# Performance work log

Measured on AMD Instinct MI355X. Metric: run time of the kernel, lower is better.

Reference implementation:

```python
import jax, jax.numpy as jnp
import numpy as np

CLASS_NUM = 20
C_FEAT = 256
STRIDE = 16
ROI = 7
SCALE = 1.0 / 16.0
TOPK = 300
NMS_THR = 0.7
SCORE_THR = 0.5
SAMPLES = 2  # nearest samples per bin edge in roi_pool


def _conv(x, W, b, stride, padding):
    y = jax.lax.conv_general_dilated(x, W, (stride, stride), padding,
                                     dimension_numbers=('NCHW', 'OIHW', 'NCHW'))
    return y + b[None, :, None, None]


def _pairwise_iou(boxes):
    x1, y1, x2, y2 = boxes[:, 0], boxes[:, 1], boxes[:, 2], boxes[:, 3]
    area = jnp.maximum(x2 - x1, 0.) * jnp.maximum(y2 - y1, 0.)
    ix1 = jnp.maximum(x1[:, None], x1[None, :])
    iy1 = jnp.maximum(y1[:, None], y1[None, :])
    ix2 = jnp.minimum(x2[:, None], x2[None, :])
    iy2 = jnp.minimum(y2[:, None], y2[None, :])
    inter = jnp.maximum(ix2 - ix1, 0.) * jnp.maximum(iy2 - iy1, 0.)
    return inter / jnp.maximum(area[:, None] + area[None, :] - inter, 1e-6)


def _nms(boxes, scores, valid, thr):
    # fixed-size greedy NMS: returns boolean keep mask aligned with input order
    K = boxes.shape[0]
    order = jnp.argsort(-scores)
    b = boxes[order]
    v = valid[order]
    iou = _pairwise_iou(b)  # [K,K]
    idx = jnp.arange(K)

    def body(i, keep):
        k = keep[i] & v[i]
        suppress = (iou[i] > thr) & (idx > i) & k
        return keep & (~suppress)

    keep = jax.lax.fori_loop(0, K, body, v)
    return jnp.zeros((K,), bool).at[order].set(keep)


def _roi_pool(f, boxes):
    # f: [C,H,W] feature map; boxes: [K,4] in image coords.
    # Max pool over ROI x SAMPLES nearest-neighbor samples per bin (jit-safe roi_pool).
    C, H, W = f.shape
    K = boxes.shape[0]
    b = boxes * SCALE
    frac = (jnp.arange(ROI)[:, None] + (jnp.arange(SAMPLES)[None, :] + 0.5) / SAMPLES).reshape(-1) / ROI
    xs = b[:, 0:1] + frac[None, :] * (b[:, 2:3] - b[:, 0:1])  # [K, ROI*S]
    ys = b[:, 1:2] + frac[None, :] * (b[:, 3:4] - b[:, 1:2])
    ix = jnp.clip(jnp.floor(xs), 0, W - 1).astype(jnp.int32)
    iy = jnp.clip(jnp.floor(ys), 0, H - 1).astype(jnp.int32)
    g = f[:, iy[:, :, None], ix[:, None, :]]  # [C,K,ROI*S,ROI*S]
    g = g.reshape(C, K, ROI, SAMPLES, ROI, SAMPLES)
    return g.max(axis=(3, 5)).transpose(1, 0, 2, 3)  # [K,C,ROI,ROI]


def setup_inputs() -> dict:
    key = jax.random.key(0)
    ks = jax.random.split(key, 12)
    img = 800
    x = jax.random.uniform(ks[0], (1, 3, img, img), jnp.float32)
    gt_boxes = jax.random.uniform(ks[1], (8, 5), jnp.float32) * img

    def w_(k, shape, fan_in):
        return jax.random.normal(k, shape, jnp.float32) * (1.0 / np.sqrt(fan_in))

    d_flat = ROI * ROI * C_FEAT
    return {
        'x': x, 'gt_boxes': gt_boxes,
        'W_feat': w_(ks[2], (C_FEAT, 3, STRIDE, STRIDE), 3 * STRIDE * STRIDE),
        'b_feat': jnp.zeros((C_FEAT,), jnp.float32),
        'W1': w_(ks[3], (C_FEAT, C_FEAT, 3, 3), C_FEAT * 9),
        'b1': jnp.zeros((C_FEAT,), jnp.float32),
        'Wc': w_(ks[4], (2, C_FEAT), C_FEAT),
        'bc': jnp.zeros((2,), jnp.float32),
        'Wb': w_(ks[5], (4, C_FEAT), C_FEAT),
        'bb': jnp.zeros((4,), jnp.float32),
        'fc1_w': w_(ks[6], (4096, d_flat), d_flat),
        'fc1_b': jnp.zeros((4096,), jnp.float32),
        'fc2_w': w_(ks[7], (4096, 4096), 4096),
        'fc2_b': jnp.zeros((4096,), jnp.float32),
        'cls_w': w_(ks[8], (CLASS_NUM + 1, 4096), 4096),
        'cls_b': jnp.zeros((CLASS_NUM + 1,), jnp.float32),
        'box_w': w_(ks[9], (4, 4096), 4096),
        'box_b': jnp.zeros((4,), jnp.float32),
        'w': 800, 'h': 800,
    }


def reference(x, gt_boxes, W_feat, b_feat, W1, b1, Wc, bc, Wb, bb,
              fc1_w, fc1_b, fc2_w, fc2_b, cls_w, cls_b, box_w, box_b, w, h):
    feature = _conv(x, W_feat, b_feat, STRIDE, 'VALID')          # [1,C,50,50]
    hmap = jax.nn.relu(_conv(feature, W1, b1, 1, 'SAME'))
    pre_labels = (jnp.einsum('nchw,oc->nhwo', hmap, Wc) + bc).reshape(-1, 2)
    pre_boxes = (jnp.einsum('nchw,oc->nhwo', hmap, Wb) + bb).reshape(-1, 4)
    logits = jax.nn.softmax(pre_labels, axis=-1)[:, 1]           # [2500]
    scores, idx = jax.lax.top_k(logits, TOPK)                    # fixed-size stand-in for score>thr select
    valid = scores > SCORE_THR
    pb = pre_boxes[idx]
    wf = jnp.float32(w)
    hf = jnp.float32(h)
    # box decode exactly as the original per-box loop (vectorized)
    x1 = jnp.maximum(pb[:, 2] - pb[:, 0] / 2, 0.)
    y1 = jnp.maximum(pb[:, 3] - pb[:, 1] / 2, 0.)
    x2 = jnp.minimum(pb[:, 2] + pb[:, 0], wf)
    y2 = jnp.minimum(pb[:, 3] + pb[:, 1], hf)
    boxes = jnp.stack([x1, y1, x2, y2], axis=-1)                 # [K,4]
    keep = _nms(boxes, scores, valid, NMS_THR)
    pooled = _roi_pool(feature[0], boxes)                        # [K,C,7,7]
    flat = pooled.reshape(TOPK, -1)
    h1 = jax.nn.relu(flat @ fc1_w.T + fc1_b)
    h2 = jax.nn.relu(h1 @ fc2_w.T + fc2_b)
    cls = h2 @ cls_w.T + cls_b                                   # [K,21]
    box = h2 @ box_w.T + box_b                                   # [K,4]
    out = jnp.where(keep[:, None], jnp.concatenate([cls, box], axis=-1), 0.)
    return out                                                   # [K,25]
```

## Files before the change

kernel.cpp:

```cpp
#include <hip/hip_runtime.h>
#include <hip/hip_bf16.h>
#include <math.h>

#define NPIX   2500
#define CFEAT  256
#define NTOP   300
#define DFLAT  12544
#define FCN    4096
#define FPSTRIDE 3328
#define KG1    392
#define KG2    128
#define MT     20

typedef _Float16 f16x8 __attribute__((ext_vector_type(8)));
typedef float    f32x4 __attribute__((ext_vector_type(4)));

static constexpr size_t OFF_FPAD  = 0;
static constexpr size_t OFF_HMAP  = 0x340000;
static constexpr size_t OFF_SCORE = 0x5C0000;
static constexpr size_t OFF_PREB  = 0x5D0000;
static constexpr size_t OFF_TS    = 0x5E0000;
static constexpr size_t OFF_TI    = 0x5E1000;
static constexpr size_t OFF_KEEP  = 0x5E5000;
static constexpr size_t OFF_IX    = 0x5E6000;
static constexpr size_t OFF_IY    = 0x5EB000;
static constexpr size_t OFF_AFRAG = 0x600000;
static constexpr size_t OFF_H1F   = 0xE00000;
static constexpr size_t OFF_H2    = 0x1100000;
static constexpr size_t OFF_W1T   = 0x1600000;
static constexpr size_t OFF_PART  = 0x1900000;

__device__ inline float decode_dim(const void* p) {
    int iv = *(const int*)p;
    if (iv > 0 && iv < (1 << 20)) return (float)iv;
    return __int_as_float(iv);
}

__global__ void zero_fpad(float* __restrict__ fpad) {
    int i = blockIdx.x * 256 + threadIdx.x;
    if (i < 212992) *(float4*)(fpad + (size_t)i * 4) = make_float4(0.f, 0.f, 0.f, 0.f);
}

__global__ void __launch_bounds__(256)
patch_conv(const float* __restrict__ x, const float* __restrict__ Wf,
           const float* __restrict__ bf, float* __restrict__ fpad) {
    __shared__ float w[3072];
    int co0 = blockIdx.y * 4;
    for (int t = threadIdx.x; t < 3072; t += 256) w[t] = Wf[co0 * 768 + t];
    __syncthreads();
    int p = blockIdx.x * 256 + threadIdx.x;
    if (p >= NPIX) return;
    int py = p / 50, px = p % 50;
    float acc[4];
    #pragma unroll
    for (int c = 0; c < 4; ++c) acc[c] = bf[co0 + c];
    for (int ci = 0; ci < 3; ++ci) {
        const float* xp = x + ci * 640000 + (py * 16) * 800 + px * 16;
        #pragma unroll
        for (int ky = 0; ky < 16; ++ky) {
            const float* row = xp + ky * 800;
            #pragma unroll
            for (int kq = 0; kq < 4; ++kq) {
                float4 xv = *reinterpret_cast<const float4*>(row + kq * 4);
                int kb = ci * 256 + ky * 16 + kq * 4;
                #pragma unroll
                for (int c = 0; c < 4; ++c) {
                    const float* wc = w + c * 768 + kb;
                    acc[c] += xv.x * wc[0] + xv.y * wc[1] + xv.z * wc[2] + xv.w * wc[3];
                }
            }
        }
    }
    size_t o = (size_t)(py + 1) * 64 + (px + 1);
    #pragma unroll
    for (int c = 0; c < 4; ++c) fpad[(size_t)(co0 + c) * FPSTRIDE + o] = acc[c];
}

__global__ void transpose_w1(const float* __restrict__ W1, float* __restrict__ W1t) {
    int idx = blockIdx.x * 256 + threadIdx.x;
    if (idx >= 2304 * 256) return;
    int r = idx >> 8, co = idx & 255;
    W1t[idx] = W1[co * 2304 + r];
}

__global__ void __launch_bounds__(256)
conv3x3_part(const float* __restrict__ fpad, const float* __restrict__ W1t,
             float* __restrict__ cpart) {
    int co = threadIdx.x;
    int xb = blockIdx.x * 8;
    int y  = blockIdx.y;
    int z  = blockIdx.z;
    float acc[8];
    #pragma unroll
    for (int p = 0; p < 8; ++p) acc[p] = 0.0f;
    const float* fp = fpad + (size_t)(z * 64) * FPSTRIDE + (size_t)y * 64 + xb;
    const float* wp = W1t + (size_t)(z * 64) * 9 * 256 + co;
    #pragma unroll 2
    for (int ci = 0; ci < 64; ++ci) {
        float v[3][12];
        #pragma unroll
        for (int dy = 0; dy < 3; ++dy) {
            #pragma unroll
            for (int q = 0; q < 3; ++q) {
                float4 r4 = *(const float4*)(fp + dy * 64 + q * 4);
                v[dy][q * 4 + 0] = r4.x; v[dy][q * 4 + 1] = r4.y;
                v[dy][q * 4 + 2] = r4.z; v[dy][q * 4 + 3] = r4.w;
            }
        }
        float wv[9];
        #pragma unroll
        for (int k = 0; k < 9; ++k) wv[k] = wp[k * 256];
        #pragma unroll
        for (int dy = 0; dy < 3; ++dy)
            #pragma unroll
            for (int dx = 0; dx < 3; ++dx) {
                float wvv = wv[dy * 3 + dx];
                #pragma unroll
                for (int p = 0; p < 8; ++p)
                    acc[p] += v[dy][p + dx] * wvv;
            }
        fp += FPSTRIDE;
        wp += 9 * 256;
    }
    size_t base = (size_t)z * (NPIX * 256) + (size_t)(y * 50 + xb) * 256 + co;
    #pragma unroll
    for (int p = 0; p < 8; ++p)
        if (xb + p < 50) cpart[base + (size_t)p * 256] = acc[p];
}

__global__ void reduce_conv(const float* __restrict__ cpart, const float* __restrict__ b1,
                            float* __restrict__ hmap) {
    int i = blockIdx.x * 256 + threadIdx.x;
    if (i >= NPIX * 256 / 4) return;
    float4 s = *(const float4*)(cpart + (size_t)i * 4);
    #pragma unroll
    for (int z = 1; z < 4; ++z) {
        float4 v = *(const float4*)(cpart + (size_t)z * (NPIX * 256) + (size_t)i * 4);
        s.x += v.x; s.y += v.y; s.z += v.z; s.w += v.w;
    }
    float4 b = *(const float4*)(b1 + (i & 63) * 4);
    s.x = fmaxf(s.x + b.x, 0.f); s.y = fmaxf(s.y + b.y, 0.f);
    s.z = fmaxf(s.z + b.z, 0.f); s.w = fmaxf(s.w + b.w, 0.f);
    *(float4*)(hmap + (size_t)i * 4) = s;
}

__global__ void head_k(const float* __restrict__ hmap, const float* __restrict__ Wc,
                       const float* __restrict__ bc, const float* __restrict__ Wb,
                       const float* __restrict__ bb, float* __restrict__ score,
                       float* __restrict__ preb) {
    int lane = threadIdx.x & 63;
    int p = blockIdx.x * 4 + (threadIdx.x >> 6);
    if (p >= NPIX) return;
    float4 h  = *(const float4*)(hmap + (size_t)p * 256 + lane * 4);
    float4 c0 = *(const float4*)(Wc + lane * 4);
    float4 c1 = *(const float4*)(Wc + 256 + lane * 4);
    float4 w0 = *(const float4*)(Wb + lane * 4);
    float4 w1 = *(const float4*)(Wb + 256 + lane * 4);
    float4 w2 = *(const float4*)(Wb + 512 + lane * 4);
    float4 w3 = *(const float4*)(Wb + 768 + lane * 4);
    float s[6];
    s[0] = h.x*c0.x + h.y*c0.y + h.z*c0.z + h.w*c0.w;
    s[1] = h.x*c1.x + h.y*c1.y + h.z*c1.z + h.w*c1.w;
    s[2] = h.x*w0.x + h.y*w0.y + h.z*w0.z + h.w*w0.w;
    s[3] = h.x*w1.x + h.y*w1.y + h.z*w1.z + h.w*w1.w;
    s[4] = h.x*w2.x + h.y*w2.y + h.z*w2.z + h.w*w2.w;
    s[5] = h.x*w3.x + h.y*w3.y + h.z*w3.z + h.w*w3.w;
    #pragma unroll
    for (int o = 1; o < 64; o <<= 1) {
        #pragma unroll
        for (int q = 0; q < 6; ++q) s[q] += __shfl_xor(s[q], o, 64);
    }
    if (lane == 0) {
        float s0 = s[0] + bc[0], s1 = s[1] + bc[1];
        float m = fmaxf(s0, s1);
        float e0 = expf(s0 - m), e1 = expf(s1 - m);
        score[p] = e1 / (e0 + e1);
        preb[p * 4 + 0] = s[2] + bb[0];
        preb[p * 4 + 1] = s[3] + bb[1];
        preb[p * 4 + 2] = s[4] + bb[2];
        preb[p * 4 + 3] = s[5] + bb[3];
    }
}

__global__ void __launch_bounds__(1024) topk_k(const float* __restrict__ score,
                                               float* __restrict__ ts, int* __restrict__ ti) {
    __shared__ float sv[4096];
    __shared__ int   si[4096];
    int tid = threadIdx.x;
    for (int t = tid; t < 4096; t += 1024) {
        sv[t] = (t < NPIX) ? score[t] : -INFINITY;
        si[t] = t;
    }
    __syncthreads();
    for (int k = 2; k <= 4096; k <<= 1) {
        for (int j = k >> 1; j > 0; j >>= 1) {
            for (int t = tid; t < 4096; t += 1024) {
                int l = t ^ j;
                if (l > t) {
                    float vt = sv[t], vl = sv[l];
                    int it = si[t], il = si[l];
                    bool l_before_t = (vl > vt) || (vl == vt && il < it);
                    bool dir = ((t & k) == 0);
                    if (dir == l_before_t) {
                        sv[t] = vl; sv[l] = vt;
                        si[t] = il; si[l] = it;
                    }
                }
            }
            __syncthreads();
        }
    }
    for (int t = tid; t < NTOP; t += 1024) { ts[t] = sv[t]; ti[t] = si[t]; }
}

__global__ void __launch_bounds__(320)
nms_fused(const float* __restrict__ preb, const int* __restrict__ ti,
          const float* __restrict__ ts, const void* wp_, const void* hp_,
          int* __restrict__ keep, int* __restrict__ ixb, int* __restrict__ iyb) {
    __shared__ float X1[320], Y1[320], X2[320], Y2[320], AR[320];
    __shared__ unsigned long long MASK[320][5];
    __shared__ unsigned long long KEEPW[5];
    int t = threadIdx.x;
    int lane = t & 63;
    int w = t >> 6;

    float x1 = 0.f, y1 = 0.f, x2 = 0.f, y2 = 0.f;
    bool v = false;
    if (t < NTOP) {
        float wf = decode_dim(wp_), hf = decode_dim(hp_);
        int id = ti[t];
        float p0 = preb[id * 4 + 0], p1 = preb[id * 4 + 1];
        float p2 = preb[id * 4 + 2], p3 = preb[id * 4 + 3];
        x1 = fmaxf(p2 - p0 * 0.5f, 0.0f);
        y1 = fmaxf(p3 - p1 * 0.5f, 0.0f);
        x2 = fminf(p2 + p0, wf);
        y2 = fminf(p3 + p1, hf);
        v = ts[t] > 0.5f;
        float bx1 = x1 * 0.0625f, by1 = y1 * 0.0625f;
        float bx2 = x2 * 0.0625f, by2 = y2 * 0.0625f;
        #pragma unroll
        for (int m = 0; m < 14; ++m) {
            int i = m >> 1, s = m & 1;
            float frac = ((float)i + (s ? 0.75f : 0.25f)) / 7.0f;
            float xs = bx1 + frac * (bx2 - bx1);
            float ys = by1 + frac * (by2 - by1);
            float fx = floorf(xs); fx = fminf(fmaxf(fx, 0.0f), 49.0f);
            float fy = floorf(ys); fy = fminf(fmaxf(fy, 0.0f), 49.0f);
            ixb[t * 14 + m] = (int)fx;
            iyb[t * 14 + m] = (int)fy;
        }
    }
    X1[t] = x1; Y1[t] = y1; X2[t] = x2; Y2[t] = y2;
    AR[t] = fmaxf(x2 - x1, 0.0f) * fmaxf(y2 - y1, 0.0f);
    unsigned long long vb = __ballot(v);
    if (lane == 0) KEEPW[w] = vb;
    __syncthreads();

    float xi1 = X1[t], yi1 = Y1[t], xi2 = X2[t], yi2 = Y2[t], ai = AR[t];
    #pragma unroll
    for (int jw = 0; jw < 5; ++jw) {
        unsigned long long mword = 0ull;
        #pragma unroll 4
        for (int j2 = 0; j2 < 64; ++j2) {
            int j = jw * 64 + j2;
            float ix1 = fmaxf(xi1, X1[j]);
            float iy1 = fmaxf(yi1, Y1[j]);
            float ix2 = fminf(xi2, X2[j]);
            float iy2 = fminf(yi2, Y2[j]);
            float inter = fmaxf(ix2 - ix1, 0.0f) * fmaxf(iy2 - iy1, 0.0f);
            float iou = inter / fmaxf(ai + AR[j] - inter, 1e-6f);
            bool sup = (iou > 0.7f) && (j > t) && (j < NTOP);
            mword |= sup ? (1ull << j2) : 0ull;
        }
        MASK[t][jw] = mword;
    }
    __syncthreads();
    if (w != 0) return;

    unsigned long long m[5][5];
    #pragma unroll
    for (int g = 0; g < 5; ++g)
        #pragma unroll
        for (int q = 0; q < 5; ++q)
            m[g][q] = MASK[g * 64 + lane][q];
    unsigned long long kw0 = KEEPW[0], kw1 = KEEPW[1], kw2 = KEEPW[2],
                       kw3 = KEEPW[3], kw4 = KEEPW[4];
    #pragma unroll
    for (int g = 0; g < 5; ++g) {
        for (int i2 = 0; i2 < 64; ++i2) {
            unsigned long long kg = (g == 0) ? kw0 : (g == 1) ? kw1 :
                                    (g == 2) ? kw2 : (g == 3) ? kw3 : kw4;
            bool alive = (kg >> i2) & 1ull;
            unsigned long long b0 = __shfl(m[g][0], i2, 64);
            unsigned long long b1 = __shfl(m[g][1], i2, 64);
            unsigned long long b2 = __shfl(m[g][2], i2, 64);
            unsigned long long b3 = __shfl(m[g][3], i2, 64);
            unsigned long long b4 = __shfl(m[g][4], i2, 64);
            if (alive) {
                kw0 &= ~b0; kw1 &= ~b1; kw2 &= ~b2; kw3 &= ~b3; kw4 &= ~b4;
            }
        }
    }
    #pragma unroll
    for (int g = 0; g < 5; ++g) {
        unsigned long long kg = (g == 0) ? kw0 : (g == 1) ? kw1 :
                                (g == 2) ? kw2 : (g == 3) ? kw3 : kw4;
        int j = g * 64 + lane;
        if (j < NTOP) keep[j] = (int)((kg >> lane) & 1ull);
    }
}

__global__ void __launch_bounds__(256)
roipool_frag(const float* __restrict__ fpad, const int* __restrict__ ixb,
             const int* __restrict__ iyb, _Float16* __restrict__ Af) {
    int wid = blockIdx.x * 256 + threadIdx.x;
    if (wid >= MT * KG1 * 64) return;
    int l = wid & 63;
    int g = (wid >> 6) % KG1;
    int T = wid / (KG1 * 64);
    int mm = T * 16 + (l & 15);
    int kbase = g * 32 + ((l >> 4) & 3) * 8;
    union { _Float16 h[8]; uint4 u; } o;
    if (mm < NTOP) {
        const int* ix = ixb + mm * 14;
        const int* iy = iyb + mm * 14;
        #pragma unroll
        for (int e = 0; e < 8; ++e) {
            int k = kbase + e;
            int c = k / 49, ij = k % 49, i = ij / 7, jx = ij % 7;
            int y0 = iy[2 * i] + 1, y1 = iy[2 * i + 1] + 1;
            int x0 = ix[2 * jx] + 1, x1 = ix[2 * jx + 1] + 1;
            const float* f = fpad + (size_t)c * FPSTRIDE;
            float v = fmaxf(fmaxf(f[y0 * 64 + x0], f[y0 * 64 + x1]),
                            fmaxf(f[y1 * 64 + x0], f[y1 * 64 + x1]));
            o.h[e] = (_Float16)v;
        }
    } else {
        o.u.x = 0u; o.u.y = 0u; o.u.z = 0u; o.u.w = 0u;
    }
    *(uint4*)(Af + (size_t)wid * 8) = o.u;
}

__global__ void __launch_bounds__(512)
gemm_fullm(const _Float16* __restrict__ Af, const float* __restrict__ B,
           float* __restrict__ part, int K, int KG, int kchunk) {
    __shared__ char Bs[64 * 128];
    int tid = threadIdx.x;
    int lane = tid & 63;
    int w = tid >> 6;
    int wm = w & 3, wn = w >> 2;
    int n0 = blockIdx.x * 64;
    int ks = blockIdx.y * kchunk;

    f32x4 acc[5][2];
    #pragma unroll
    for (int tm = 0; tm < 5; ++tm)
        #pragma unroll
        for (int tn = 0; tn < 2; ++tn)
            acc[tm][tn] = f32x4{0.f, 0.f, 0.f, 0.f};

    int srow = tid >> 3;
    int skp  = (tid & 7) * 8;
    const float* bsrc = B + (size_t)(n0 + srow) * K + ks + skp;
    int sboff = srow * 128 + ((skp * 2) ^ ((srow & 7) << 4));

    float4 v0 = *(const float4*)(bsrc);
    float4 v1 = *(const float4*)(bsrc + 4);
    for (int k0 = 0; k0 < kchunk; k0 += 64) {
        union { _Float16 h[8]; uint4 u; } cv;
        cv.h[0] = (_Float16)v0.x; cv.h[1] = (_Float16)v0.y;
        cv.h[2] = (_Float16)v0.z; cv.h[3] = (_Float16)v0.w;
        cv.h[4] = (_Float16)v1.x; cv.h[5] = (_Float16)v1.y;
        cv.h[6] = (_Float16)v1.z; cv.h[7] = (_Float16)v1.w;
        __syncthreads();
        *(uint4*)(Bs + sboff) = cv.u;
        __syncthreads();
        if (k0 + 64 < kchunk) {
            v0 = *(const float4*)(bsrc + k0 + 64);
            v1 = *(const float4*)(bsrc + k0 + 68);
        }
        #pragma unroll
        for (int kk = 0; kk < 2; ++kk) {
            int g = (ks + k0 + kk * 32) >> 5;
            f16x8 bfr[2];
            #pragma unroll
            for (int tn = 0; tn < 2; ++tn) {
                int row = wn * 32 + tn * 16 + (lane & 15);
                int kb = kk * 64 + (lane >> 4) * 16;
                bfr[tn] = *(const f16x8*)(Bs + row * 128 + (kb ^ ((row & 7) << 4)));
            }
            #pragma unroll
            for (int tm = 0; tm < 5; ++tm) {
                int T = wm * 5 + tm;
                f16x8 a = *(const f16x8*)(Af + ((size_t)(T * KG + g) * 64 + lane) * 8);
                #pragma unroll
                for (int tn = 0; tn < 2; ++tn)
                    acc[tm][tn] = __builtin_amdgcn_mfma_f32_16x16x32_f16(a, bfr[tn], acc[tm][tn], 0, 0, 0);
            }
        }
    }
    float* pout = part + (size_t)blockIdx.y * (NTOP * FCN);
    #pragma unroll
    for (int tm = 0; tm < 5; ++tm) {
        int mbase = (wm * 5 + tm) * 16 + (lane >> 4) * 4;
        #pragma unroll
        for (int j = 0; j < 4; ++j) {
            int m = mbase + j;
            if (m < NTOP) {
                #pragma unroll
                for (int tn = 0; tn < 2; ++tn) {
                    int n = n0 + wn * 32 + tn * 16 + (lane & 15);
                    pout[(size_t)m * FCN + n] = acc[tm][tn][j];
                }
            }
        }
    }
}

__global__ void reduce_fc1(const float* __restrict__ part, const float* __restrict__ bias,
                           _Float16* __restrict__ h1f, int ns) {
    int i = blockIdx.x * 256 + threadIdx.x;
    if (i >= NTOP * 512) return;
    int m = i >> 9;
    int f = (i & 511) * 8;
    float s[8];
    const float* p0 = part + (size_t)m * FCN + f;
    #pragma unroll
    for (int e = 0; e < 8; ++e) s[e] = p0[e];
    for (int z = 1; z < ns; ++z) {
        const float* pz = p0 + (size_t)z * (NTOP * FCN);
        #pragma unroll
        for (int e = 0; e < 8; ++e) s[e] += pz[e];
    }
    union { _Float16 h[8]; uint4 u; } o;
    #pragma unroll
    for (int e = 0; e < 8; ++e) o.h[e] = (_Float16)fmaxf(s[e] + bias[f + e], 0.0f);
    int T = m >> 4, g = f >> 5, l = (m & 15) + 16 * ((f >> 3) & 3);
    *(uint4*)(h1f + ((size_t)(T * KG2 + g) * 64 + l) * 8) = o.u;
}

__global__ void reduce_fc2(const float* __restrict__ part, const float* __restrict__ bias,
                           float* __restrict__ outp, int ns) {
    size_t i = (size_t)blockIdx.x * 256 + threadIdx.x;
    size_t mn4 = (size_t)NTOP * FCN / 4;
    if (i >= mn4) return;
    float4 s = *(const float4*)(part + i * 4);
    for (int zz = 1; zz < ns; ++zz) {
        float4 v = *(const float4*)(part + (size_t)zz * (NTOP * FCN) + i * 4);
        s.x += v.x; s.y += v.y; s.z += v.z; s.w += v.w;
    }
    int n = (int)((i * 4) % FCN);
    float4 b = *(const float4*)(bias + n);
    s.x = fmaxf(s.x + b.x, 0.f); s.y = fmaxf(s.y + b.y, 0.f);
    s.z = fmaxf(s.z + b.z, 0.f); s.w = fmaxf(s.w + b.w, 0.f);
    *(float4*)(outp + i * 4) = s;
}

__global__ void __launch_bounds__(256)
final_k(const float* __restrict__ h2, const float* __restrict__ clsw,
        const float* __restrict__ clsb, const float* __restrict__ boxw,
        const float* __restrict__ boxb, const int* __restrict__ keep,
        float* __restrict__ out) {
    int gid = blockIdx.x * 4 + (threadIdx.x >> 6);
    if (gid >= NTOP * 25) return;
    int lane = threadIdx.x & 63;
    int k = gid / 25, o = gid % 25;
    const float* w;
    float b;
    if (o < 21) { w = clsw + (size_t)o * 4096; b = clsb[o]; }
    else        { w = boxw + (size_t)(o - 21) * 4096; b = boxb[o - 21]; }
    const float* h = h2 + (size_t)k * 4096;
    float s = 0.0f;
    #pragma unroll
    for (int i = 0; i < 16; ++i) {
        float4 hv = *(const float4*)(h + (i * 64 + lane) * 4);
        float4 wv = *(const float4*)(w + (i * 64 + lane) * 4);
        s += hv.x * wv.x + hv.y * wv.y + hv.z * wv.z + hv.w * wv.w;
    }
    #pragma unroll
    for (int off = 1; off < 64; off <<= 1) s += __shfl_xor(s, off, 64);
    if (lane == 0) out[gid] = keep[k] ? (s + b) : 0.0f;
}

extern "C" void kernel_launch(void* const* d_in, const int* in_sizes, int n_in,
                              void* d_out, int out_size, void* d_ws, size_t ws_size,
                              hipStream_t stream) {
    const float* x    = (const float*)d_in[0];
    const float* Wf   = (const float*)d_in[2];
    const float* bf   = (const float*)d_in[3];
    const float* W1   = (const float*)d_in[4];
    const float* b1   = (const float*)d_in[5];
    const float* Wc   = (const float*)d_in[6];
    const float* bc   = (const float*)d_in[7];
    const float* Wb   = (const float*)d_in[8];
    const float* bb   = (const float*)d_in[9];
    const float* fc1w = (const float*)d_in[10];
    const float* fc1b = (const float*)d_in[11];
    const float* fc2w = (const float*)d_in[12];
    const float* fc2b = (const float*)d_in[13];
    const float* clsw = (const float*)d_in[14];
    const float* clsb = (const float*)d_in[15];
    const float* boxw = (const float*)d_in[16];
    const float* boxb = (const float*)d_in[17];
    const void*  wp   = d_in[18];
    const void*  hp   = d_in[19];

    char* ws = (char*)d_ws;
    float*     fpad  = (float*)(ws + OFF_FPAD);
    float*     hmap  = (float*)(ws + OFF_HMAP);
    float*     score = (float*)(ws + OFF_SCORE);
    float*     preb  = (float*)(ws + OFF_PREB);
    float*     ts    = (float*)(ws + OFF_TS);
    int*       ti    = (int*)(ws + OFF_TI);
    int*       keep  = (int*)(ws + OFF_KEEP);
    int*       ixb   = (int*)(ws + OFF_IX);
    int*       iyb   = (int*)(ws + OFF_IY);
    _Float16*  Af    = (_Float16*)(ws + OFF_AFRAG);
    float*     cpart = (float*)(ws + OFF_AFRAG);
    _Float16*  h1f   = (_Float16*)(ws + OFF_H1F);
    float*     h2    = (float*)(ws + OFF_H2);
    float*     w1t   = (float*)(ws + OFF_W1T);
    float*     out   = (float*)d_out;

    size_t slot = (size_t)NTOP * FCN * 4;
    size_t avail = ws_size > OFF_PART ? (ws_size - OFF_PART) / slot : 0;
    int ns1 = (avail >= 7) ? 7 : (avail >= 4) ? 4 : (avail >= 2) ? 2 : 1;
    int ns2 = (avail >= 4) ? 4 : (avail >= 2) ? 2 : 1;
    float* part1 = (avail >= 1) ? (float*)(ws + OFF_PART) : h2;
    float* part2 = (avail >= 1) ? (float*)(ws + OFF_PART) : (float*)Af;
    int kch1 = (196 / ns1) * 64;
    int kch2 = (64 / ns2) * 64;

    zero_fpad<<<832, 256, 0, stream>>>(fpad);
    patch_conv<<<dim3(10, 64), 256, 0, stream>>>(x, Wf, bf, fpad);
    transpose_w1<<<(2304 * 256 + 255) / 256, 256, 0, stream>>>(W1, w1t);
    conv3x3_part<<<dim3(7, 50, 4), 256, 0, stream>>>(fpad, w1t, cpart);
    reduce_conv<<<(NPIX * 256 / 4 + 255) / 256, 256, 0, stream>>>(cpart, b1, hmap);
    head_k<<<625, 256, 0, stream>>>(hmap, Wc, bc, Wb, bb, score, preb);
    topk_k<<<1, 1024, 0, stream>>>(score, ts, ti);
    nms_fused<<<1, 320, 0, stream>>>(preb, ti, ts, wp, hp, keep, ixb, iyb);
    roipool_frag<<<(MT * KG1 * 64 + 255) / 256, 256, 0, stream>>>(fpad, ixb, iyb, Af);
    gemm_fullm<<<dim3(64, ns1), 512, 0, stream>>>(Af, fc1w, part1, DFLAT, KG1, kch1);
    reduce_fc1<<<(NTOP * 512 + 255) / 256, 256, 0, stream>>>(part1, fc1b, h1f, ns1);
    gemm_fullm<<<dim3(64, ns2), 512, 0, stream>>>(h1f, fc2w, part2, FCN, KG2, kch2);
    reduce_fc2<<<(NTOP * FCN / 4 + 255) / 256, 256, 0, stream>>>(part2, fc2b, h2, ns2);
    final_k<<<(NTOP * 25 + 3) / 4, 256, 0, stream>>>(h2, clsw, clsb, boxw, boxb, keep, out);
}
```

Measured before the change: 427.6 us.

## Fuse conv reduce with head, topk with NMS, double-buffer GEMM B tiles

Measured after the change: 408.1 us. 4.6% less time.

```diff
diff --git a/kernel.cpp b/kernel.cpp
--- a/kernel.cpp
+++ b/kernel.cpp
@@ -16,11 +16,8 @@
 typedef float    f32x4 __attribute__((ext_vector_type(4)));
 
 static constexpr size_t OFF_FPAD  = 0;
-static constexpr size_t OFF_HMAP  = 0x340000;
 static constexpr size_t OFF_SCORE = 0x5C0000;
 static constexpr size_t OFF_PREB  = 0x5D0000;
-static constexpr size_t OFF_TS    = 0x5E0000;
-static constexpr size_t OFF_TI    = 0x5E1000;
 static constexpr size_t OFF_KEEP  = 0x5E5000;
 static constexpr size_t OFF_IX    = 0x5E6000;
 static constexpr size_t OFF_IY    = 0x5EB000;
@@ -85,7 +82,7 @@
 
 __global__ void __launch_bounds__(256)
 conv3x3_part(const float* __restrict__ fpad, const float* __restrict__ W1t,
-             float* __restrict__ cpart) {
+             float* __restrict__ cpart, int zci) {
     int co = threadIdx.x;
     int xb = blockIdx.x * 8;
     int y  = blockIdx.y;
@@ -93,10 +90,10 @@
     float acc[8];
     #pragma unroll
     for (int p = 0; p < 8; ++p) acc[p] = 0.0f;
-    const float* fp = fpad + (size_t)(z * 64) * FPSTRIDE + (size_t)y * 64 + xb;
-    const float* wp = W1t + (size_t)(z * 64) * 9 * 256 + co;
+    const float* fp = fpad + (size_t)(z * zci) * FPSTRIDE + (size_t)y * 64 + xb;
+    const float* wp = W1t + (size_t)(z * zci) * 9 * 256 + co;
     #pragma unroll 2
-    for (int ci = 0; ci < 64; ++ci) {
+    for (int ci = 0; ci < zci; ++ci) {
         float v[3][12];
         #pragma unroll
         for (int dy = 0; dy < 3; ++dy) {
@@ -128,30 +125,23 @@
         if (xb + p < 50) cpart[base + (size_t)p * 256] = acc[p];
 }
 
-__global__ void reduce_conv(const float* __restrict__ cpart, const float* __restrict__ b1,
-                            float* __restrict__ hmap) {
-    int i = blockIdx.x * 256 + threadIdx.x;
-    if (i >= NPIX * 256 / 4) return;
-    float4 s = *(const float4*)(cpart + (size_t)i * 4);
-    #pragma unroll
-    for (int z = 1; z < 4; ++z) {
-        float4 v = *(const float4*)(cpart + (size_t)z * (NPIX * 256) + (size_t)i * 4);
-        s.x += v.x; s.y += v.y; s.z += v.z; s.w += v.w;
-    }
-    float4 b = *(const float4*)(b1 + (i & 63) * 4);
-    s.x = fmaxf(s.x + b.x, 0.f); s.y = fmaxf(s.y + b.y, 0.f);
-    s.z = fmaxf(s.z + b.z, 0.f); s.w = fmaxf(s.w + b.w, 0.f);
-    *(float4*)(hmap + (size_t)i * 4) = s;
-}
-
-__global__ void head_k(const float* __restrict__ hmap, const float* __restrict__ Wc,
-                       const float* __restrict__ bc, const float* __restrict__ Wb,
-                       const float* __restrict__ bb, float* __restrict__ score,
-                       float* __restrict__ preb) {
+__global__ void __launch_bounds__(256)
+reducehead_k(const float* __restrict__ cpart, const float* __restrict__ b1,
+             const float* __restrict__ Wc, const float* __restrict__ bc,
+             const float* __restrict__ Wb, const float* __restrict__ bb,
+             float* __restrict__ score, float* __restrict__ preb, int zs) {
     int lane = threadIdx.x & 63;
     int p = blockIdx.x * 4 + (threadIdx.x >> 6);
     if (p >= NPIX) return;
-    float4 h  = *(const float4*)(hmap + (size_t)p * 256 + lane * 4);
+    size_t off = (size_t)p * 256 + lane * 4;
+    float4 h = *(const float4*)(cpart + off);
+    for (int z = 1; z < zs; ++z) {
+        float4 v = *(const float4*)(cpart + (size_t)z * (NPIX * 256) + off);
+        h.x += v.x; h.y += v.y; h.z += v.z; h.w += v.w;
+    }
+    float4 b = *(const float4*)(b1 + lane * 4);
+    h.x = fmaxf(h.x + b.x, 0.f); h.y = fmaxf(h.y + b.y, 0.f);
+    h.z = fmaxf(h.z + b.z, 0.f); h.w = fmaxf(h.w + b.w, 0.f);
     float4 c0 = *(const float4*)(Wc + lane * 4);
     float4 c1 = *(const float4*)(Wc + 256 + lane * 4);
     float4 w0 = *(const float4*)(Wb + lane * 4);
@@ -182,11 +172,19 @@
     }
 }
 
-__global__ void __launch_bounds__(1024) topk_k(const float* __restrict__ score,
-                                               float* __restrict__ ts, int* __restrict__ ti) {
+__global__ void __launch_bounds__(1024)
+topknms_k(const float* __restrict__ score, const float* __restrict__ preb,
+          const void* wp_, const void* hp_, int* __restrict__ keep,
+          int* __restrict__ ixb, int* __restrict__ iyb) {
     __shared__ float sv[4096];
     __shared__ int   si[4096];
+    __shared__ float X1[320], Y1[320], X2[320], Y2[320], AR[320];
+    __shared__ unsigned long long MASK[320][5];
+    __shared__ unsigned long long KEEPW[5];
     int tid = threadIdx.x;
+    int lane = tid & 63;
+    int w = tid >> 6;
+
     for (int t = tid; t < 4096; t += 1024) {
         sv[t] = (t < NPIX) ? score[t] : -INFINITY;
         si[t] = t;
@@ -210,103 +208,95 @@
             __syncthreads();
         }
     }
-    for (int t = tid; t < NTOP; t += 1024) { ts[t] = sv[t]; ti[t] = si[t]; }
-}
-
-__global__ void __launch_bounds__(320)
-nms_fused(const float* __restrict__ preb, const int* __restrict__ ti,
-          const float* __restrict__ ts, const void* wp_, const void* hp_,
-          int* __restrict__ keep, int* __restrict__ ixb, int* __restrict__ iyb) {
-    __shared__ float X1[320], Y1[320], X2[320], Y2[320], AR[320];
-    __shared__ unsigned long long MASK[320][5];
-    __shared__ unsigned long long KEEPW[5];
-    int t = threadIdx.x;
-    int lane = t & 63;
-    int w = t >> 6;
-
-    float x1 = 0.f, y1 = 0.f, x2 = 0.f, y2 = 0.f;
-    bool v = false;
-    if (t < NTOP) {
-        float wf = decode_dim(wp_), hf = decode_dim(hp_);
-        int id = ti[t];
-        float p0 = preb[id * 4 + 0], p1 = preb[id * 4 + 1];
-        float p2 = preb[id * 4 + 2], p3 = preb[id * 4 + 3];
-        x1 = fmaxf(p2 - p0 * 0.5f, 0.0f);
-        y1 = fmaxf(p3 - p1 * 0.5f, 0.0f);
-        x2 = fminf(p2 + p0, wf);
-        y2 = fminf(p3 + p1, hf);
-        v = ts[t] > 0.5f;
-        float bx1 = x1 * 0.0625f, by1 = y1 * 0.0625f;
-        float bx2 = x2 * 0.0625f, by2 = y2 * 0.0625f;
-        #pragma unroll
-        for (int m = 0; m < 14; ++m) {
-            int i = m >> 1, s = m & 1;
-            float frac = ((float)i + (s ? 0.75f : 0.25f)) / 7.0f;
-            float xs = bx1 + frac * (bx2 - bx1);
-            float ys = by1 + frac * (by2 - by1);
-            float fx = floorf(xs); fx = fminf(fmaxf(fx, 0.0f), 49.0f);
-            float fy = floorf(ys); fy = fminf(fmaxf(fy, 0.0f), 49.0f);
-            ixb[t * 14 + m] = (int)fx;
-            iyb[t * 14 + m] = (int)fy;
-        }
-    }
-    X1[t] = x1; Y1[t] = y1; X2[t] = x2; Y2[t] = y2;
-    AR[t] = fmaxf(x2 - x1, 0.0f) * fmaxf(y2 - y1, 0.0f);
-    unsigned long long vb = __ballot(v);
-    if (lane == 0) KEEPW[w] = vb;
+
+    if (tid < 320) {
+        float x1 = 0.f, y1 = 0.f, x2 = 0.f, y2 = 0.f;
+        bool v = false;
+        if (tid < NTOP) {
+            float wf = decode_dim(wp_), hf = decode_dim(hp_);
+            int id = si[tid];
+            float p0 = preb[id * 4 + 0], p1 = preb[id * 4 + 1];
+            float p2 = preb[id * 4 + 2], p3 = preb[id * 4 + 3];
+            x1 = fmaxf(p2 - p0 * 0.5f, 0.0f);
+            y1 = fmaxf(p3 - p1 * 0.5f, 0.0f);
+            x2 = fminf(p2 + p0, wf);
+            y2 = fminf(p3 + p1, hf);
+            v = sv[tid] > 0.5f;
+            float bx1 = x1 * 0.0625f, by1 = y1 * 0.0625f;
+            float bx2 = x2 * 0.0625f, by2 = y2 * 0.0625f;
+            #pragma unroll
+            for (int m = 0; m < 14; ++m) {
+                int i = m >> 1, s = m & 1;
+                float frac = ((float)i + (s ? 0.75f : 0.25f)) / 7.0f;
+                float xs = bx1 + frac * (bx2 - bx1);
+                float ys = by1 + frac * (by2 - by1);
+                float fx = floorf(xs); fx = fminf(fmaxf(fx, 0.0f), 49.0f);
+                float fy = floorf(ys); fy = fminf(fmaxf(fy, 0.0f), 49.0f);
+                ixb[tid * 14 + m] = (int)fx;
+                iyb[tid * 14 + m] = (int)fy;
+            }
+        }
+        X1[tid] = x1; Y1[tid] = y1; X2[tid] = x2; Y2[tid] = y2;
+        AR[tid] = fmaxf(x2 - x1, 0.0f) * fmaxf(y2 - y1, 0.0f);
+        unsigned long long vb = __ballot(v);
+        if (lane == 0) KEEPW[w] = vb;
+    }
     __syncthreads();
 
-    float xi1 = X1[t], yi1 = Y1[t], xi2 = X2[t], yi2 = Y2[t], ai = AR[t];
-    #pragma unroll
-    for (int jw = 0; jw < 5; ++jw) {
-        unsigned long long mword = 0ull;
-        #pragma unroll 4
-        for (int j2 = 0; j2 < 64; ++j2) {
-            int j = jw * 64 + j2;
-            float ix1 = fmaxf(xi1, X1[j]);
-            float iy1 = fmaxf(yi1, Y1[j]);
-            float ix2 = fminf(xi2, X2[j]);
-            float iy2 = fminf(yi2, Y2[j]);
-            float inter = fmaxf(ix2 - ix1, 0.0f) * fmaxf(iy2 - iy1, 0.0f);
-            float iou = inter / fmaxf(ai + AR[j] - inter, 1e-6f);
-            bool sup = (iou > 0.7f) && (j > t) && (j < NTOP);
-            mword |= sup ? (1ull << j2) : 0ull;
-        }
-        MASK[t][jw] = mword;
+    if (tid < 320) {
+        float xi1 = X1[tid], yi1 = Y1[tid], xi2 = X2[tid], yi2 = Y2[tid], ai = AR[tid];
+        #pragma unroll
+        for (int jw = 0; jw < 5; ++jw) {
+            unsigned long long mword = 0ull;
+            #pragma unroll 4
+            for (int j2 = 0; j2 < 64; ++j2) {
+                int j = jw * 64 + j2;
+                float ix1 = fmaxf(xi1, X1[j]);
+                float iy1 = fmaxf(yi1, Y1[j]);
+                float ix2 = fminf(xi2, X2[j]);
+                float iy2 = fminf(yi2, Y2[j]);
+                float inter = fmaxf(ix2 - ix1, 0.0f) * fmaxf(iy2 - iy1, 0.0f);
+                float iou = inter / fmaxf(ai + AR[j] - inter, 1e-6f);
+                bool sup = (iou > 0.7f) && (j > tid) && (j < NTOP);
+                mword |= sup ? (1ull << j2) : 0ull;
+            }
+            MASK[tid][jw] = mword;
+        }
     }
     __syncthreads();
-    if (w != 0) return;
-
-    unsigned long long m[5][5];
-    #pragma unroll
-    for (int g = 0; g < 5; ++g)
-        #pragma unroll
-        for (int q = 0; q < 5; ++q)
-            m[g][q] = MASK[g * 64 + lane][q];
-    unsigned long long kw0 = KEEPW[0], kw1 = KEEPW[1], kw2 = KEEPW[2],
-                       kw3 = KEEPW[3], kw4 = KEEPW[4];
-    #pragma unroll
-    for (int g = 0; g < 5; ++g) {
-        for (int i2 = 0; i2 < 64; ++i2) {
+
+    if (tid < 64) {
+        unsigned long long m[5][5];
+        #pragma unroll
+        for (int g = 0; g < 5; ++g)
+            #pragma unroll
+            for (int q = 0; q < 5; ++q)
+                m[g][q] = MASK[g * 64 + lane][q];
+        unsigned long long kw0 = KEEPW[0], kw1 = KEEPW[1], kw2 = KEEPW[2],
+                           kw3 = KEEPW[3], kw4 = KEEPW[4];
+        #pragma unroll
+        for (int g = 0; g < 5; ++g) {
+            for (int i2 = 0; i2 < 64; ++i2) {
+                unsigned long long kg = (g == 0) ? kw0 : (g == 1) ? kw1 :
+                                        (g == 2) ? kw2 : (g == 3) ? kw3 : kw4;
+                bool alive = (kg >> i2) & 1ull;
+                unsigned long long b0 = __shfl(m[g][0], i2, 64);
+                unsigned long long b1 = __shfl(m[g][1], i2, 64);
+                unsigned long long b2 = __shfl(m[g][2], i2, 64);
+                unsigned long long b3 = __shfl(m[g][3], i2, 64);
+                unsigned long long b4 = __shfl(m[g][4], i2, 64);
+                if (alive) {
+                    kw0 &= ~b0; kw1 &= ~b1; kw2 &= ~b2; kw3 &= ~b3; kw4 &= ~b4;
+                }
+            }
+        }
+        #pragma unroll
+        for (int g = 0; g < 5; ++g) {
             unsigned long long kg = (g == 0) ? kw0 : (g == 1) ? kw1 :
                                     (g == 2) ? kw2 : (g == 3) ? kw3 : kw4;
-            bool alive = (kg >> i2) & 1ull;
-            unsigned long long b0 = __shfl(m[g][0], i2, 64);
-            unsigned long long b1 = __shfl(m[g][1], i2, 64);
-            unsigned long long b2 = __shfl(m[g][2], i2, 64);
-            unsigned long long b3 = __shfl(m[g][3], i2, 64);
-            unsigned long long b4 = __shfl(m[g][4], i2, 64);
-            if (alive) {
-                kw0 &= ~b0; kw1 &= ~b1; kw2 &= ~b2; kw3 &= ~b3; kw4 &= ~b4;
-            }
-        }
-    }
-    #pragma unroll
-    for (int g = 0; g < 5; ++g) {
-        unsigned long long kg = (g == 0) ? kw0 : (g == 1) ? kw1 :
-                                (g == 2) ? kw2 : (g == 3) ? kw3 : kw4;
-        int j = g * 64 + lane;
-        if (j < NTOP) keep[j] = (int)((kg >> lane) & 1ull);
+            int j = g * 64 + lane;
+            if (j < NTOP) keep[j] = (int)((kg >> lane) & 1ull);
+        }
     }
 }
 
@@ -344,13 +334,14 @@
 __global__ void __launch_bounds__(512)
 gemm_fullm(const _Float16* __restrict__ Af, const float* __restrict__ B,
            float* __restrict__ part, int K, int KG, int kchunk) {
-    __shared__ char Bs[64 * 128];
+    __shared__ char Bs[2][64 * 128];
     int tid = threadIdx.x;
     int lane = tid & 63;
     int w = tid >> 6;
     int wm = w & 3, wn = w >> 2;
     int n0 = blockIdx.x * 64;
     int ks = blockIdx.y * kchunk;
+    int nt = kchunk >> 6;
 
     f32x4 acc[5][2];
     #pragma unroll
@@ -366,28 +357,43 @@
 
     float4 v0 = *(const float4*)(bsrc);
     float4 v1 = *(const float4*)(bsrc + 4);
-    for (int k0 = 0; k0 < kchunk; k0 += 64) {
+    {
         union { _Float16 h[8]; uint4 u; } cv;
         cv.h[0] = (_Float16)v0.x; cv.h[1] = (_Float16)v0.y;
         cv.h[2] = (_Float16)v0.z; cv.h[3] = (_Float16)v0.w;
         cv.h[4] = (_Float16)v1.x; cv.h[5] = (_Float16)v1.y;
         cv.h[6] = (_Float16)v1.z; cv.h[7] = (_Float16)v1.w;
-        __syncthreads();
-        *(uint4*)(Bs + sboff) = cv.u;
-        __syncthreads();
-        if (k0 + 64 < kchunk) {
-            v0 = *(const float4*)(bsrc + k0 + 64);
-            v1 = *(const float4*)(bsrc + k0 + 68);
+        *(uint4*)(Bs[0] + sboff) = cv.u;
+    }
+    if (nt > 1) {
+        v0 = *(const float4*)(bsrc + 64);
+        v1 = *(const float4*)(bsrc + 68);
+    }
+    __syncthreads();
+
+    for (int k0 = 0; k0 < nt; ++k0) {
+        const char* cur = Bs[k0 & 1];
+        if (k0 + 1 < nt) {
+            union { _Float16 h[8]; uint4 u; } cv;
+            cv.h[0] = (_Float16)v0.x; cv.h[1] = (_Float16)v0.y;
+            cv.h[2] = (_Float16)v0.z; cv.h[3] = (_Float16)v0.w;
+            cv.h[4] = (_Float16)v1.x; cv.h[5] = (_Float16)v1.y;
+            cv.h[6] = (_Float16)v1.z; cv.h[7] = (_Float16)v1.w;
+            *(uint4*)(Bs[(k0 + 1) & 1] + sboff) = cv.u;
+            if (k0 + 2 < nt) {
+                v0 = *(const float4*)(bsrc + (k0 + 2) * 64);
+                v1 = *(const float4*)(bsrc + (k0 + 2) * 64 + 4);
+            }
         }
         #pragma unroll
         for (int kk = 0; kk < 2; ++kk) {
-            int g = (ks + k0 + kk * 32) >> 5;
+            int g = (ks + k0 * 64 + kk * 32) >> 5;
             f16x8 bfr[2];
             #pragma unroll
             for (int tn = 0; tn < 2; ++tn) {
                 int row = wn * 32 + tn * 16 + (lane & 15);
                 int kb = kk * 64 + (lane >> 4) * 16;
-                bfr[tn] = *(const f16x8*)(Bs + row * 128 + (kb ^ ((row & 7) << 4)));
+                bfr[tn] = *(const f16x8*)(cur + row * 128 + (kb ^ ((row & 7) << 4)));
             }
             #pragma unroll
             for (int tm = 0; tm < 5; ++tm) {
@@ -398,6 +404,7 @@
                     acc[tm][tn] = __builtin_amdgcn_mfma_f32_16x16x32_f16(a, bfr[tn], acc[tm][tn], 0, 0, 0);
             }
         }
+        __syncthreads();
     }
     float* pout = part + (size_t)blockIdx.y * (NTOP * FCN);
     #pragma unroll
@@ -507,16 +514,12 @@
 
     char* ws = (char*)d_ws;
     float*     fpad  = (float*)(ws + OFF_FPAD);
-    float*     hmap  = (float*)(ws + OFF_HMAP);
     float*     score = (float*)(ws + OFF_SCORE);
     float*     preb  = (float*)(ws + OFF_PREB);
-    float*     ts    = (float*)(ws + OFF_TS);
-    int*       ti    = (int*)(ws + OFF_TI);
     int*       keep  = (int*)(ws + OFF_KEEP);
     int*       ixb   = (int*)(ws + OFF_IX);
     int*       iyb   = (int*)(ws + OFF_IY);
     _Float16*  Af    = (_Float16*)(ws + OFF_AFRAG);
-    float*     cpart = (float*)(ws + OFF_AFRAG);
     _Float16*  h1f   = (_Float16*)(ws + OFF_H1F);
     float*     h2    = (float*)(ws + OFF_H2);
     float*     w1t   = (float*)(ws + OFF_W1T);
@@ -530,15 +533,15 @@
     float* part2 = (avail >= 1) ? (float*)(ws + OFF_PART) : (float*)Af;
     int kch1 = (196 / ns1) * 64;
     int kch2 = (64 / ns2) * 64;
+    int zs = (avail >= 5) ? 8 : 4;
+    float* cpart = (avail >= 5) ? (float*)(ws + OFF_PART) : (float*)(ws + OFF_AFRAG);
 
     zero_fpad<<<832, 256, 0, stream>>>(fpad);
     patch_conv<<<dim3(10, 64), 256, 0, stream>>>(x, Wf, bf, fpad);
     transpose_w1<<<(2304 * 256 + 255) / 256, 256, 0, stream>>>(W1, w1t);
-    conv3x3_part<<<dim3(7, 50, 4), 256, 0, stream>>>(fpad, w1t, cpart);
-    reduce_conv<<<(NPIX * 256 / 4 + 255) / 256, 256, 0, stream>>>(cpart, b1, hmap);
-    head_k<<<625, 256, 0, stream>>>(hmap, Wc, bc, Wb, bb, score, preb);
-    topk_k<<<1, 1024, 0, stream>>>(score, ts, ti);
-    nms_fused<<<1, 320, 0, stream>>>(preb, ti, ts, wp, hp, keep, ixb, iyb);
+    conv3x3_part<<<dim3(7, 50, zs), 256, 0, stream>>>(fpad, w1t, cpart, 256 / zs);
+    reducehead_k<<<625, 256, 0, stream>>>(cpart, b1, Wc, bc, Wb, bb, score, preb, zs);
+    topknms_k<<<1, 1024, 0, stream>>>(score, preb, wp, hp, keep, ixb, iyb);
     roipool_frag<<<(MT * KG1 * 64 + 255) / 256, 256, 0, stream>>>(fpad, ixb, iyb, Af);
     gemm_fullm<<<dim3(64, ns1), 512, 0, stream>>>(Af, fc1w, part1, DFLAT, KG1, kch1);
     reduce_fc1<<<(NTOP * 512 + 255) / 256, 256, 0, stream>>>(part1, fc1b, h1f, ns1);
```
